# Performance work log

Hardware: AMD Instinct MI355X
Metric: run time of the kernel (lower is better)

Reference implementation:

```python
import jax, jax.numpy as jnp
import numpy as np

N, L, E, H = 4, 2048, 1024, 16
DK = E // H  # 64

def setup_inputs() -> dict:
    key = jax.random.key(0)
    ks = jax.random.split(key, 5)
    scale = 0.02
    return {
        "x": jax.random.normal(ks[0], (N, L, E), dtype=jnp.float32),
        "Wq": jax.random.normal(ks[1], (E, E), dtype=jnp.float32) * scale,
        "Wk": jax.random.normal(ks[2], (E, E), dtype=jnp.float32) * scale,
        "Wv": jax.random.normal(ks[3], (E, E), dtype=jnp.float32) * scale,
        "Wo": jax.random.normal(ks[4], (E, E), dtype=jnp.float32) * scale,
    }

def reference(x, Wq, Wk, Wv, Wo):
    n, l, _ = x.shape
    # nn.Linear(bias=False): y = x @ W.T
    q = x @ Wq.T  # (n, l, H*DK)
    k = x @ Wk.T
    v = x @ Wv.T
    # Faithful to torch .view: plain reshape (NOT transpose-based head split)
    q = q.reshape(n, H, l, DK)
    k = k.reshape(n, H, l, DK)
    v = v.reshape(n, H, l, DK)
    scores = jnp.einsum('nhqd,nhkd->nhqk', q, k) / jnp.sqrt(jnp.float32(DK))
    attn = jax.nn.softmax(scores, axis=-1)
    out = jnp.einsum('nhqk,nhkd->nhqd', attn, v).reshape(n, l, H * DK)
    return out @ Wo.T
```

## Files before the change

### kernel.cpp

```cpp
#include <hip/hip_runtime.h>


#define DEVI __device__ __forceinline__

typedef _Float16 half8 __attribute__((ext_vector_type(8)));
typedef _Float16 half4 __attribute__((ext_vector_type(4)));
typedef float f32x4 __attribute__((ext_vector_type(4)));

DEVI void gload_lds16(const void* g, void* l) {
    __builtin_amdgcn_global_load_lds(
        (const __attribute__((address_space(1))) void*)g,
        (__attribute__((address_space(3))) void*)l,
        16, 0, 0);
}

DEVI f32x4 zero4() { f32x4 z = {0.f, 0.f, 0.f, 0.f}; return z; }

#if __has_builtin(__builtin_amdgcn_exp2f)
DEVI float fast_exp2(float x) { return __builtin_amdgcn_exp2f(x); }
#else
DEVI float fast_exp2(float x) { return exp2f(x); }
#endif

#if __has_builtin(__builtin_amdgcn_mfma_f32_16x16x16f16)
DEVI f32x4 mfma16(half4 a, half4 b, f32x4 c) {
    return __builtin_amdgcn_mfma_f32_16x16x16f16(a, b, c, 0, 0, 0);
}
#else
DEVI f32x4 mfma16(half4 a, half4 b, f32x4 c) {
    asm volatile("v_mfma_f32_16x16x16_f16 %0, %1, %2, %0"
                 : "+v"(c) : "v"(a), "v"(b));
    return c;
}
#endif

DEVI half8 lds_read8_swz(const _Float16* base, int row, int colbyte) {
    const char* p = (const char*)base;
    const int off = (row * 128 + colbyte) ^ ((row & 7) << 4);
    return *(const half8*)(p + off);
}
DEVI half4 lds_read4_swz(const _Float16* base, int row, int colbyte) {
    const char* p = (const char*)base;
    const int off = (row * 128 + colbyte) ^ ((row & 7) << 4);
    return *(const half4*)(p + off);
}

__global__ __launch_bounds__(256) void f2h_kernel(const float* __restrict__ s,
                                                  _Float16* __restrict__ d) {
    const size_t i = (size_t)blockIdx.x * 256 + threadIdx.x;
    const float4 v = ((const float4*)s)[i];
    half4 h;
    h[0] = (_Float16)v.x; h[1] = (_Float16)v.y;
    h[2] = (_Float16)v.z; h[3] = (_Float16)v.w;
    ((half4*)d)[i] = h;
}

template<int MODE>
__global__ __launch_bounds__(256) void gemm_k(const _Float16* __restrict__ A,
                                              const _Float16* __restrict__ B,
                                              void* __restrict__ Cout,
                                              float qscale) {
    constexpr int NBLK = (MODE == 0) ? 24 : 8;
    constexpr int CPX  = (MODE == 0) ? 192 : 64;
    alignas(16) __shared__ _Float16 As[128 * 64];
    alignas(16) __shared__ _Float16 Bs[128 * 64];
    const int t = threadIdx.x;
    const int lane = t & 63;
    const int w = t >> 6;
    const int wr = (w >> 1) * 64;
    const int wc = (w & 1) * 64;
    const int nid = (blockIdx.x & 7) * CPX + (blockIdx.x >> 3);
    const int bn = (nid % NBLK) * 128;
    const int bm = (nid / NBLK) * 128;
    const int r16 = lane & 15;
    const int q4 = lane >> 4;
    const int sr = t >> 3;
    const int sc8 = (t & 7) * 8;

    f32x4 acc[4][4];
    #pragma unroll
    for (int mi = 0; mi < 4; ++mi)
        #pragma unroll
        for (int ni = 0; ni < 4; ++ni)
            acc[mi][ni] = zero4();

    for (int kt = 0; kt < 1024; kt += 64) {
        #pragma unroll
        for (int i = 0; i < 4; ++i) {
            gload_lds16(A + (size_t)(bm + i * 32 + sr) * 1024 + kt + sc8, &As[i * 2048 + t * 8]);
            gload_lds16(B + (size_t)(bn + i * 32 + sr) * 1024 + kt + sc8, &Bs[i * 2048 + t * 8]);
        }
        __syncthreads();
        #pragma unroll
        for (int kk = 0; kk < 2; ++kk) {
            half8 a[4], b[4];
            #pragma unroll
            for (int mi = 0; mi < 4; ++mi)
                a[mi] = *(const half8*)&As[(wr + mi * 16 + r16) * 64 + kk * 32 + q4 * 8];
            #pragma unroll
            for (int ni = 0; ni < 4; ++ni)
                b[ni] = *(const half8*)&Bs[(wc + ni * 16 + r16) * 64 + kk * 32 + q4 * 8];
            #pragma unroll
            for (int mi = 0; mi < 4; ++mi)
                #pragma unroll
                for (int ni = 0; ni < 4; ++ni)
                    acc[mi][ni] = __builtin_amdgcn_mfma_f32_16x16x32_f16(a[mi], b[ni], acc[mi][ni], 0, 0, 0);
        }
        __syncthreads();
    }
    if (MODE == 0) {
        const int which = bn >> 10;
        const int cb = bn & 1023;
        const float alpha = (which == 0) ? qscale : 1.0f;
        _Float16* C = (_Float16*)Cout + (size_t)which * 8388608;
        #pragma unroll
        for (int mi = 0; mi < 4; ++mi) {
            const int row = bm + wr + mi * 16 + q4 * 4;
            #pragma unroll
            for (int ni = 0; ni < 4; ++ni) {
                const int col = cb + wc + ni * 16 + r16;
                #pragma unroll
                for (int i = 0; i < 4; ++i)
                    C[(size_t)(row + i) * 1024 + col] = (_Float16)(acc[mi][ni][i] * alpha);
            }
        }
    } else {
        float* C = (float*)Cout;
        #pragma unroll
        for (int mi = 0; mi < 4; ++mi) {
            const int row = bm + wr + mi * 16 + q4 * 4;
            #pragma unroll
            for (int ni = 0; ni < 4; ++ni) {
                const int col = bn + wc + ni * 16 + r16;
                #pragma unroll
                for (int i = 0; i < 4; ++i)
                    C[(size_t)(row + i) * 1024 + col] = acc[mi][ni][i];
            }
        }
    }
}

__global__ __launch_bounds__(256) void transpose_v(const _Float16* __restrict__ V,
                                                   _Float16* __restrict__ Vt) {
    __shared__ unsigned short lds[64 * 65];
    const int t = threadIdx.x;
    const int kt = blockIdx.x;
    const size_t hb = (size_t)blockIdx.y * 131072;
    const int r = t >> 2;
    const int c0 = (t & 3) * 16;
    const unsigned short* Vi = (const unsigned short*)V;
    #pragma unroll
    for (int j = 0; j < 2; ++j) {
        union { uint4 u; unsigned short s[8]; } tmp;
        tmp.u = *(const uint4*)&Vi[hb + (size_t)(kt * 64 + r) * 64 + c0 + j * 8];
        #pragma unroll
        for (int e = 0; e < 8; ++e)
            lds[r * 65 + c0 + j * 8 + e] = tmp.s[e];
    }
    __syncthreads();
    unsigned short* Vo = (unsigned short*)Vt;
    #pragma unroll
    for (int j = 0; j < 16; ++j) {
        const int idx = j * 256 + t;
        const int d = idx >> 6;
        const int c = idx & 63;
        Vo[hb + (size_t)d * 2048 + kt * 64 + c] = lds[c * 65 + d];
    }
}

__global__ __launch_bounds__(256) void attn_kernel(const _Float16* __restrict__ Q,
                                                   const _Float16* __restrict__ K,
                                                   const _Float16* __restrict__ Vt,
                                                   _Float16* __restrict__ O) {
    alignas(16) __shared__ _Float16 Ks[2][64 * 64];
    alignas(16) __shared__ _Float16 Vs[2][64 * 64];
    const int t = threadIdx.x;
    const int lane = t & 63;
    const int w = t >> 6;
    const int nid = (blockIdx.x & 7) * 128 + (blockIdx.x >> 3);
    const size_t hb = (size_t)(nid >> 4) * 131072;
    const int qt = nid & 15;
    const int r16 = lane & 15;
    const int q4 = lane >> 4;
    const int sr = t >> 3;
    const int sc = t & 7;

    half8 aq[2][2];
    const int q0 = qt * 128 + w * 32;
    #pragma unroll
    for (int mi = 0; mi < 2; ++mi)
        #pragma unroll
        for (int kk = 0; kk < 2; ++kk)
            aq[mi][kk] = *(const half8*)&Q[hb + (size_t)(q0 + mi * 16 + r16) * 64 + kk * 32 + q4 * 8];

    f32x4 o[4][2];
    float lsum[2] = {0.f, 0.f};
    #pragma unroll
    for (int ni = 0; ni < 4; ++ni)
        #pragma unroll
        for (int mi = 0; mi < 2; ++mi)
            o[ni][mi] = zero4();

    const int R0 = sr, R1 = 32 + sr;
    const int scs0 = (sc ^ (R0 & 7)) * 8;
    const int scs1 = (sc ^ (R1 & 7)) * 8;

    {
        gload_lds16(&K[hb + (size_t)R0 * 64 + scs0],        &Ks[0][t * 8]);
        gload_lds16(&K[hb + (size_t)R1 * 64 + scs1],        &Ks[0][2048 + t * 8]);
        gload_lds16(&Vt[hb + (size_t)R0 * 2048 + scs0],     &Vs[0][t * 8]);
        gload_lds16(&Vt[hb + (size_t)R1 * 2048 + scs1],     &Vs[0][2048 + t * 8]);
    }
    __syncthreads();

    int pb = 0;
    for (int kt = 0; kt < 32; ++kt) {
        if (kt + 1 < 32) {
            const size_t kb = hb + (size_t)(kt + 1) * 64 * 64;
            gload_lds16(&K[kb + (size_t)R0 * 64 + scs0],                 &Ks[pb ^ 1][t * 8]);
            gload_lds16(&K[kb + (size_t)R1 * 64 + scs1],                 &Ks[pb ^ 1][2048 + t * 8]);
            gload_lds16(&Vt[hb + (size_t)R0 * 2048 + (kt + 1) * 64 + scs0], &Vs[pb ^ 1][t * 8]);
            gload_lds16(&Vt[hb + (size_t)R1 * 2048 + (kt + 1) * 64 + scs1], &Vs[pb ^ 1][2048 + t * 8]);
        }

        f32x4 sT[4][2];
        #pragma unroll
        for (int ki = 0; ki < 4; ++ki)
            #pragma unroll
            for (int mi = 0; mi < 2; ++mi)
                sT[ki][mi] = zero4();
        __builtin_amdgcn_s_setprio(1);
        #pragma unroll
        for (int kk = 0; kk < 2; ++kk) {
            half8 ak[4];
            #pragma unroll
            for (int ki = 0; ki < 4; ++ki)
                ak[ki] = lds_read8_swz(Ks[pb], ki * 16 + r16, (kk * 32 + q4 * 8) * 2);
            #pragma unroll
            for (int ki = 0; ki < 4; ++ki)
                #pragma unroll
                for (int mi = 0; mi < 2; ++mi)
                    sT[ki][mi] = __builtin_amdgcn_mfma_f32_16x16x32_f16(ak[ki], aq[mi][kk], sT[ki][mi], 0, 0, 0);
        }
        __builtin_amdgcn_s_setprio(0);

        half4 pT[4][2];
        #pragma unroll
        for (int ki = 0; ki < 4; ++ki)
            #pragma unroll
            for (int mi = 0; mi < 2; ++mi) {
                const float p0 = fast_exp2(sT[ki][mi][0]);
                const float p1 = fast_exp2(sT[ki][mi][1]);
                const float p2 = fast_exp2(sT[ki][mi][2]);
                const float p3 = fast_exp2(sT[ki][mi][3]);
                lsum[mi] += (p0 + p1) + (p2 + p3);
                half4 pv;
                pv[0] = (_Float16)p0; pv[1] = (_Float16)p1;
                pv[2] = (_Float16)p2; pv[3] = (_Float16)p3;
                pT[ki][mi] = pv;
            }

        __builtin_amdgcn_s_setprio(1);
        #pragma unroll
        for (int ki = 0; ki < 4; ++ki)
            #pragma unroll
            for (int ni = 0; ni < 4; ++ni) {
                const half4 av = lds_read4_swz(Vs[pb], ni * 16 + r16, ki * 32 + q4 * 8);
                #pragma unroll
                for (int mi = 0; mi < 2; ++mi)
                    o[ni][mi] = mfma16(av, pT[ki][mi], o[ni][mi]);
            }
        __builtin_amdgcn_s_setprio(0);

        __syncthreads();
        pb ^= 1;
    }

    float inv[2];
    #pragma unroll
    for (int mi = 0; mi < 2; ++mi) {
        float l = lsum[mi];
        l += __shfl_xor(l, 16);
        l += __shfl_xor(l, 32);
        inv[mi] = 1.f / l;
    }
    #pragma unroll
    for (int mi = 0; mi < 2; ++mi) {
        const int q = q0 + mi * 16 + r16;
        #pragma unroll
        for (int ni = 0; ni < 4; ++ni) {
            half4 ov;
            #pragma unroll
            for (int i = 0; i < 4; ++i)
                ov[i] = (_Float16)(o[ni][mi][i] * inv[mi]);
            *(half4*)&O[hb + (size_t)q * 64 + ni * 16 + q4 * 4] = ov;
        }
    }
}

extern "C" void kernel_launch(void* const* d_in, const int* in_sizes, int n_in,
                              void* d_out, int out_size, void* d_ws, size_t ws_size,
                              hipStream_t stream) {
    const float* x  = (const float*)d_in[0];
    const float* Wq = (const float*)d_in[1];
    const float* Wk = (const float*)d_in[2];
    const float* Wv = (const float*)d_in[3];
    const float* Wo = (const float*)d_in[4];

    const size_t XSZ = (size_t)8192 * 1024;
    const size_t WSZ = (size_t)1024 * 1024;

    _Float16* ws  = (_Float16*)d_ws;
    _Float16* xh  = ws;
    _Float16* wqh = ws + XSZ;
    _Float16* wkh = wqh + WSZ;
    _Float16* wvh = wkh + WSZ;
    _Float16* woh = wvh + WSZ;
    _Float16* qh  = woh + WSZ;
    _Float16* kh  = qh + XSZ;
    _Float16* vh  = kh + XSZ;
    _Float16* aoh = vh + XSZ;
    _Float16* vth = xh;

    f2h_kernel<<<XSZ / 4 / 256, 256, 0, stream>>>(x,  xh);
    f2h_kernel<<<WSZ / 4 / 256, 256, 0, stream>>>(Wq, wqh);
    f2h_kernel<<<WSZ / 4 / 256, 256, 0, stream>>>(Wk, wkh);
    f2h_kernel<<<WSZ / 4 / 256, 256, 0, stream>>>(Wv, wvh);
    f2h_kernel<<<WSZ / 4 / 256, 256, 0, stream>>>(Wo, woh);

    const float qscale = 0.125f * 1.44269504088896340736f;

    gemm_k<0><<<1536, 256, 0, stream>>>(xh, wqh, (void*)qh, qscale);

    transpose_v<<<dim3(32, 64), 256, 0, stream>>>(vh, vth);

    attn_kernel<<<1024, 256, 0, stream>>>(qh, kh, vth, aoh);

    gemm_k<1><<<512, 256, 0, stream>>>(aoh, woh, d_out, 1.0f);
    (void)in_sizes; (void)n_in; (void)out_size; (void)ws_size;
}
```

Before: 305.9 us.

## Double-buffer GEMM with 512-thread 256x128 tiles and repack V for contiguous tile loads

The GEMM kernel now uses 512-thread blocks with 256x128 output tiles, double-buffered LDS stages prefetched via global_load_lds, explicit vmcnt waits, XOR-swizzled LDS layout and raised wave priority during the MFMA section. The V transpose is replaced by a repack into a per-tile layout, so attention loads each V tile with contiguous 16-byte loads and reads it from LDS with simple unswizzled half4 loads. The goal is to hide global-load latency behind MFMA work in the projections and to cut strided V traffic in attention. The cost is more LDS per block (96 KB), fewer blocks, and possible LDS bank conflicts on the new unswizzled V reads.

```diff
diff --git a/kernel.cpp b/kernel.cpp
--- a/kernel.cpp
+++ b/kernel.cpp
@@ -38,11 +38,6 @@
     const char* p = (const char*)base;
     const int off = (row * 128 + colbyte) ^ ((row & 7) << 4);
     return *(const half8*)(p + off);
-}
-DEVI half4 lds_read4_swz(const _Float16* base, int row, int colbyte) {
-    const char* p = (const char*)base;
-    const int off = (row * 128 + colbyte) ^ ((row & 7) << 4);
-    return *(const half4*)(p + off);
 }
 
 __global__ __launch_bounds__(256) void f2h_kernel(const float* __restrict__ s,
@@ -56,26 +51,25 @@
 }
 
 template<int MODE>
-__global__ __launch_bounds__(256) void gemm_k(const _Float16* __restrict__ A,
-                                              const _Float16* __restrict__ B,
-                                              void* __restrict__ Cout,
-                                              float qscale) {
-    constexpr int NBLK = (MODE == 0) ? 24 : 8;
-    constexpr int CPX  = (MODE == 0) ? 192 : 64;
-    alignas(16) __shared__ _Float16 As[128 * 64];
-    alignas(16) __shared__ _Float16 Bs[128 * 64];
+__global__ __launch_bounds__(512, 2) void gemm2(const _Float16* __restrict__ A,
+                                                const _Float16* __restrict__ B,
+                                                void* __restrict__ Cout,
+                                                float qscale) {
+    constexpr int CPX = (MODE == 0) ? 96 : 32;
+    alignas(16) __shared__ _Float16 As[2][16384];
+    alignas(16) __shared__ _Float16 Bs[2][8192];
     const int t = threadIdx.x;
     const int lane = t & 63;
     const int w = t >> 6;
-    const int wr = (w >> 1) * 64;
-    const int wc = (w & 1) * 64;
-    const int nid = (blockIdx.x & 7) * CPX + (blockIdx.x >> 3);
-    const int bn = (nid % NBLK) * 128;
-    const int bm = (nid / NBLK) * 128;
+    const int wm = w >> 1;
+    const int wn = w & 1;
     const int r16 = lane & 15;
     const int q4 = lane >> 4;
-    const int sr = t >> 3;
-    const int sc8 = (t & 7) * 8;
+    const int nid = (blockIdx.x & 7) * CPX + (blockIdx.x >> 3);
+    const int bm = (nid & 31) * 256;
+    const int bn = (nid >> 5) * 128;
+    const int srow = t >> 3;
+    const int scol = ((t & 7) ^ (srow & 7)) * 8;
 
     f32x4 acc[4][4];
     #pragma unroll
@@ -84,41 +78,62 @@
         for (int ni = 0; ni < 4; ++ni)
             acc[mi][ni] = zero4();
 
-    for (int kt = 0; kt < 1024; kt += 64) {
-        #pragma unroll
-        for (int i = 0; i < 4; ++i) {
-            gload_lds16(A + (size_t)(bm + i * 32 + sr) * 1024 + kt + sc8, &As[i * 2048 + t * 8]);
-            gload_lds16(B + (size_t)(bn + i * 32 + sr) * 1024 + kt + sc8, &Bs[i * 2048 + t * 8]);
-        }
-        __syncthreads();
+    auto stage = [&](int b, int kt) {
+        #pragma unroll
+        for (int i = 0; i < 4; ++i)
+            gload_lds16(A + (size_t)(bm + i * 64 + srow) * 1024 + kt + scol,
+                        &As[b][i * 4096 + t * 8]);
+        #pragma unroll
+        for (int i = 0; i < 2; ++i)
+            gload_lds16(B + (size_t)(bn + i * 64 + srow) * 1024 + kt + scol,
+                        &Bs[b][i * 4096 + t * 8]);
+    };
+
+    stage(0, 0);
+    for (int it = 0; it < 16; ++it) {
+        const int cb = it & 1;
+        if (it < 15) {
+            stage(cb ^ 1, (it + 1) * 64);
+            asm volatile("s_waitcnt vmcnt(6)" ::: "memory");
+        } else {
+            asm volatile("s_waitcnt vmcnt(0)" ::: "memory");
+        }
+        __builtin_amdgcn_sched_barrier(0);
+        __builtin_amdgcn_s_barrier();
+        __builtin_amdgcn_sched_barrier(0);
+        __builtin_amdgcn_s_setprio(1);
         #pragma unroll
         for (int kk = 0; kk < 2; ++kk) {
-            half8 a[4], b[4];
+            half8 a[4], bf[4];
             #pragma unroll
             for (int mi = 0; mi < 4; ++mi)
-                a[mi] = *(const half8*)&As[(wr + mi * 16 + r16) * 64 + kk * 32 + q4 * 8];
+                a[mi] = lds_read8_swz(As[cb], wm * 64 + mi * 16 + r16, (kk * 32 + q4 * 8) * 2);
             #pragma unroll
             for (int ni = 0; ni < 4; ++ni)
-                b[ni] = *(const half8*)&Bs[(wc + ni * 16 + r16) * 64 + kk * 32 + q4 * 8];
+                bf[ni] = lds_read8_swz(Bs[cb], wn * 64 + ni * 16 + r16, (kk * 32 + q4 * 8) * 2);
             #pragma unroll
             for (int mi = 0; mi < 4; ++mi)
                 #pragma unroll
                 for (int ni = 0; ni < 4; ++ni)
-                    acc[mi][ni] = __builtin_amdgcn_mfma_f32_16x16x32_f16(a[mi], b[ni], acc[mi][ni], 0, 0, 0);
-        }
-        __syncthreads();
-    }
+                    acc[mi][ni] = __builtin_amdgcn_mfma_f32_16x16x32_f16(a[mi], bf[ni], acc[mi][ni], 0, 0, 0);
+        }
+        __builtin_amdgcn_s_setprio(0);
+        asm volatile("" ::: "memory");
+        __builtin_amdgcn_s_barrier();
+        __builtin_amdgcn_sched_barrier(0);
+    }
+
     if (MODE == 0) {
         const int which = bn >> 10;
-        const int cb = bn & 1023;
+        const int cb2 = bn & 1023;
         const float alpha = (which == 0) ? qscale : 1.0f;
         _Float16* C = (_Float16*)Cout + (size_t)which * 8388608;
         #pragma unroll
         for (int mi = 0; mi < 4; ++mi) {
-            const int row = bm + wr + mi * 16 + q4 * 4;
+            const int row = bm + wm * 64 + mi * 16 + q4 * 4;
             #pragma unroll
             for (int ni = 0; ni < 4; ++ni) {
-                const int col = cb + wc + ni * 16 + r16;
+                const int col = cb2 + wn * 64 + ni * 16 + r16;
                 #pragma unroll
                 for (int i = 0; i < 4; ++i)
                     C[(size_t)(row + i) * 1024 + col] = (_Float16)(acc[mi][ni][i] * alpha);
@@ -128,10 +143,10 @@
         float* C = (float*)Cout;
         #pragma unroll
         for (int mi = 0; mi < 4; ++mi) {
-            const int row = bm + wr + mi * 16 + q4 * 4;
+            const int row = bm + wm * 64 + mi * 16 + q4 * 4;
             #pragma unroll
             for (int ni = 0; ni < 4; ++ni) {
-                const int col = bn + wc + ni * 16 + r16;
+                const int col = bn + wn * 64 + ni * 16 + r16;
                 #pragma unroll
                 for (int i = 0; i < 4; ++i)
                     C[(size_t)(row + i) * 1024 + col] = acc[mi][ni][i];
@@ -140,8 +155,8 @@
     }
 }
 
-__global__ __launch_bounds__(256) void transpose_v(const _Float16* __restrict__ V,
-                                                   _Float16* __restrict__ Vt) {
+__global__ __launch_bounds__(256) void repack_v(const _Float16* __restrict__ V,
+                                                _Float16* __restrict__ V4) {
     __shared__ unsigned short lds[64 * 65];
     const int t = threadIdx.x;
     const int kt = blockIdx.x;
@@ -150,27 +165,35 @@
     const int c0 = (t & 3) * 16;
     const unsigned short* Vi = (const unsigned short*)V;
     #pragma unroll
-    for (int j = 0; j < 2; ++j) {
+    for (int jj = 0; jj < 2; ++jj) {
         union { uint4 u; unsigned short s[8]; } tmp;
-        tmp.u = *(const uint4*)&Vi[hb + (size_t)(kt * 64 + r) * 64 + c0 + j * 8];
+        tmp.u = *(const uint4*)&Vi[hb + (size_t)(kt * 64 + r) * 64 + c0 + jj * 8];
         #pragma unroll
         for (int e = 0; e < 8; ++e)
-            lds[r * 65 + c0 + j * 8 + e] = tmp.s[e];
+            lds[r * 65 + c0 + jj * 8 + e] = tmp.s[e];
     }
     __syncthreads();
-    unsigned short* Vo = (unsigned short*)Vt;
-    #pragma unroll
-    for (int j = 0; j < 16; ++j) {
-        const int idx = j * 256 + t;
-        const int d = idx >> 6;
-        const int c = idx & 63;
-        Vo[hb + (size_t)d * 2048 + kt * 64 + c] = lds[c * 65 + d];
+    const size_t ob = hb + (size_t)kt * 4096;
+    const unsigned short* ls = lds;
+    #pragma unroll
+    for (int h = 0; h < 2; ++h) {
+        half8 v;
+        #pragma unroll
+        for (int e = 0; e < 8; ++e) {
+            const int idx = t * 16 + h * 8 + e;
+            const int a = idx >> 8;
+            const int d = (idx >> 2) & 63;
+            const int j = idx & 3;
+            unsigned short u = ls[(4 * a + j) * 65 + d];
+            v[e] = *(const _Float16*)&u;
+        }
+        *(half8*)&V4[ob + t * 16 + h * 8] = v;
     }
 }
 
 __global__ __launch_bounds__(256) void attn_kernel(const _Float16* __restrict__ Q,
                                                    const _Float16* __restrict__ K,
-                                                   const _Float16* __restrict__ Vt,
+                                                   const _Float16* __restrict__ V4,
                                                    _Float16* __restrict__ O) {
     alignas(16) __shared__ _Float16 Ks[2][64 * 64];
     alignas(16) __shared__ _Float16 Vs[2][64 * 64];
@@ -206,21 +229,21 @@
     const int scs1 = (sc ^ (R1 & 7)) * 8;
 
     {
-        gload_lds16(&K[hb + (size_t)R0 * 64 + scs0],        &Ks[0][t * 8]);
-        gload_lds16(&K[hb + (size_t)R1 * 64 + scs1],        &Ks[0][2048 + t * 8]);
-        gload_lds16(&Vt[hb + (size_t)R0 * 2048 + scs0],     &Vs[0][t * 8]);
-        gload_lds16(&Vt[hb + (size_t)R1 * 2048 + scs1],     &Vs[0][2048 + t * 8]);
+        gload_lds16(&K[hb + (size_t)R0 * 64 + scs0],  &Ks[0][t * 8]);
+        gload_lds16(&K[hb + (size_t)R1 * 64 + scs1],  &Ks[0][2048 + t * 8]);
+        gload_lds16(&V4[hb + t * 8],                  &Vs[0][t * 8]);
+        gload_lds16(&V4[hb + 2048 + t * 8],           &Vs[0][2048 + t * 8]);
     }
     __syncthreads();
 
     int pb = 0;
     for (int kt = 0; kt < 32; ++kt) {
         if (kt + 1 < 32) {
-            const size_t kb = hb + (size_t)(kt + 1) * 64 * 64;
-            gload_lds16(&K[kb + (size_t)R0 * 64 + scs0],                 &Ks[pb ^ 1][t * 8]);
-            gload_lds16(&K[kb + (size_t)R1 * 64 + scs1],                 &Ks[pb ^ 1][2048 + t * 8]);
-            gload_lds16(&Vt[hb + (size_t)R0 * 2048 + (kt + 1) * 64 + scs0], &Vs[pb ^ 1][t * 8]);
-            gload_lds16(&Vt[hb + (size_t)R1 * 2048 + (kt + 1) * 64 + scs1], &Vs[pb ^ 1][2048 + t * 8]);
+            const size_t tb = hb + (size_t)(kt + 1) * 4096;
+            gload_lds16(&K[tb + (size_t)R0 * 64 + scs0],  &Ks[pb ^ 1][t * 8]);
+            gload_lds16(&K[tb + (size_t)R1 * 64 + scs1],  &Ks[pb ^ 1][2048 + t * 8]);
+            gload_lds16(&V4[tb + t * 8],                  &Vs[pb ^ 1][t * 8]);
+            gload_lds16(&V4[tb + 2048 + t * 8],           &Vs[pb ^ 1][2048 + t * 8]);
         }
 
         f32x4 sT[4][2];
@@ -265,7 +288,7 @@
         for (int ki = 0; ki < 4; ++ki)
             #pragma unroll
             for (int ni = 0; ni < 4; ++ni) {
-                const half4 av = lds_read4_swz(Vs[pb], ni * 16 + r16, ki * 32 + q4 * 8);
+                const half4 av = *(const half4*)&Vs[pb][(ki * 4 + q4) * 256 + (ni * 16 + r16) * 4];
                 #pragma unroll
                 for (int mi = 0; mi < 2; ++mi)
                     o[ni][mi] = mfma16(av, pT[ki][mi], o[ni][mi]);
@@ -320,7 +343,7 @@
     _Float16* kh  = qh + XSZ;
     _Float16* vh  = kh + XSZ;
     _Float16* aoh = vh + XSZ;
-    _Float16* vth = xh;
+    _Float16* v4h = xh;
 
     f2h_kernel<<<XSZ / 4 / 256, 256, 0, stream>>>(x,  xh);
     f2h_kernel<<<WSZ / 4 / 256, 256, 0, stream>>>(Wq, wqh);
@@ -330,12 +353,12 @@
 
     const float qscale = 0.125f * 1.44269504088896340736f;
 
-    gemm_k<0><<<1536, 256, 0, stream>>>(xh, wqh, (void*)qh, qscale);
-
-    transpose_v<<<dim3(32, 64), 256, 0, stream>>>(vh, vth);
-
-    attn_kernel<<<1024, 256, 0, stream>>>(qh, kh, vth, aoh);
-
-    gemm_k<1><<<512, 256, 0, stream>>>(aoh, woh, d_out, 1.0f);
+    gemm2<0><<<768, 512, 0, stream>>>(xh, wqh, (void*)qh, qscale);
+
+    repack_v<<<dim3(32, 64), 256, 0, stream>>>(vh, v4h);
+
+    attn_kernel<<<1024, 256, 0, stream>>>(qh, kh, v4h, aoh);
+
+    gemm2<1><<<256, 512, 0, stream>>>(aoh, woh, d_out, 1.0f);
     (void)in_sizes; (void)n_in; (void)out_size; (void)ws_size;
 }
```

New measurement: 317.6 us. 3.8% more time.
